# Optimization experiments

Hardware: AMD Instinct MI355X
Metric: run time of the kernel (lower is better)

## Reference

```python
import jax, jax.numpy as jnp
import numpy as np

B, Q, A, D, K = 64, 256, 256, 256, 16

def setup_inputs() -> dict:
    key = jax.random.key(0)
    k1, k2, k3, k4, k5 = jax.random.split(key, 5)
    batch_q_em = jax.random.normal(k1, (B, Q, D), dtype=jnp.float32)
    batch_da_em = jax.random.normal(k2, (B, A, D), dtype=jnp.float32)
    # xavier_uniform-style init for parameters
    lim_w = float(np.sqrt(6.0 / (D + D)))
    w = jax.random.uniform(k3, (K, D, D), minval=-lim_w, maxval=lim_w, dtype=jnp.float32)
    lim_V = float(np.sqrt(6.0 / (K + 2 * D)))
    V = jax.random.uniform(k4, (K, 2 * D), minval=-lim_V, maxval=lim_V, dtype=jnp.float32)
    lim_b = float(np.sqrt(6.0 / 2))
    b = jax.random.uniform(k5, (K, 1, 1), minval=-lim_b, maxval=lim_b, dtype=jnp.float32)
    return {"batch_q_em": batch_q_em, "batch_da_em": batch_da_em, "w": w, "V": V, "b": b}

def reference(batch_q_em, batch_da_em, w, V, b):
    Dd = batch_q_em.shape[-1]
    # bilinear term: q_i^T W_k d_j  -> [B, K, Q, A]
    first = jnp.einsum('bqd,kde,bae->bkqa', batch_q_em, w, batch_da_em)
    # linear term: V_k @ concat(q_i, d_j) == V_q @ q_i + V_d @ d_j (broadcast add)
    Vq, Vd = V[:, :Dd], V[:, Dd:]
    mid = (jnp.einsum('kd,bqd->bkq', Vq, batch_q_em)[:, :, :, None]
           + jnp.einsum('kd,bad->bka', Vd, batch_da_em)[:, :, None, :])
    return jax.nn.sigmoid(first + mid + b[None])  # b broadcasts as [1,K,1,1]
```

## Files before the change

kernel.cpp:

```cpp
#include <hip/hip_runtime.h>

typedef _Float16 h8  __attribute__((ext_vector_type(8)));
typedef _Float16 h4v __attribute__((ext_vector_type(4)));
typedef float    f32x4 __attribute__((ext_vector_type(4)));

#define QSTR 264

__global__ __launch_bounds__(256, 3)
void ntn_fused(const float* __restrict__ qg, const float* __restrict__ dg,
               const float* __restrict__ wg, const float* __restrict__ Vg,
               const float* __restrict__ bg, float* __restrict__ og)
{
    __shared__ __align__(16) _Float16 rA[64 * QSTR];
    __shared__ __align__(16) _Float16 rB[256 * 40];

    const int tid  = threadIdx.x;
    const int wv   = tid >> 6;
    const int lane = tid & 63;
    const int quad = lane >> 4;
    const int l15  = lane & 15;

    const int bid = blockIdx.x;
    const int qt = bid & 3, kk = (bid >> 2) & 15, bb = bid >> 6;

    const float* wk = wg + kk * 65536;
    const float* qb = qg + (bb * 256 + qt * 64) * 256;
    const float* db = dg + bb * 65536;
    const float* Vq = Vg + kk * 512;
    const float* Vd = Vq + 256;
    const float  bk = bg[kk];

    for (int r = 0; r < 16; ++r) {
        int f  = r * 256 + tid;
        int qq = f >> 6;
        int d4 = (f & 63) << 2;
        f32x4 v = *(const f32x4*)&qb[qq * 256 + d4];
        h4v h;
        h[0] = (_Float16)v[0]; h[1] = (_Float16)v[1];
        h[2] = (_Float16)v[2]; h[3] = (_Float16)v[3];
        *(h4v*)&rA[qq * QSTR + d4] = h;
    }

    const f32x4 zero = {0.f, 0.f, 0.f, 0.f};
    f32x4 acc[4][4];
    #pragma unroll
    for (int mt = 0; mt < 4; ++mt)
        #pragma unroll
        for (int nt = 0; nt < 4; ++nt) acc[mt][nt] = zero;

    const int e0  = (tid & 63) << 2;
    const int d0g = tid >> 6;

    for (int dc = 0; dc < 8; ++dc) {
        f32x4 Ld[8];
        #pragma unroll
        for (int r = 0; r < 8; ++r)
            Ld[r] = *(const f32x4*)&wk[(dc * 32 + d0g * 8 + r) * 256 + e0];
        #pragma unroll
        for (int i = 0; i < 4; ++i) {
            h8 hv;
            #pragma unroll
            for (int r = 0; r < 8; ++r) hv[r] = (_Float16)Ld[r][i];
            int e   = e0 + i;
            int grp = d0g ^ ((e >> 2) & 3);
            *(h8*)&rB[e * 32 + (grp << 3)] = hv;
        }
        __syncthreads();

        h8 af[4], bf[4];
        #pragma unroll
        for (int mt = 0; mt < 4; ++mt)
            af[mt] = *(const h8*)&rA[(mt * 16 + l15) * QSTR + dc * 32 + quad * 8];
        #pragma unroll
        for (int nt = 0; nt < 4; ++nt) {
            int n   = wv * 64 + nt * 16 + l15;
            int grp = quad ^ ((n >> 2) & 3);
            bf[nt] = *(const h8*)&rB[n * 32 + (grp << 3)];
        }
        #pragma unroll
        for (int mt = 0; mt < 4; ++mt)
            #pragma unroll
            for (int nt = 0; nt < 4; ++nt)
                acc[mt][nt] = __builtin_amdgcn_mfma_f32_16x16x32_f16(
                    af[mt], bf[nt], acc[mt][nt], 0, 0, 0);
        __syncthreads();
    }

    {
        float vqp = 0.f;
        int qq = tid & 63, seg = tid >> 6;
        for (int j = seg * 64; j < seg * 64 + 64; j += 8) {
            h8 hv = *(const h8*)&rA[qq * QSTR + j];
            #pragma unroll
            for (int u = 0; u < 8; ++u) vqp += (float)hv[u] * Vq[j + u];
        }
        ((float*)rB)[tid] = vqp;
    }
    __syncthreads();

    float vq_r = 0.f;
    if (tid < 64) {
        const float* fB = (const float*)rB;
        vq_r = fB[tid] + fB[tid + 64] + fB[tid + 128] + fB[tid + 192];
    }
    #pragma unroll
    for (int mt = 0; mt < 4; ++mt)
        #pragma unroll
        for (int nt = 0; nt < 4; ++nt) {
            int e = wv * 64 + nt * 16 + l15;
            #pragma unroll
            for (int reg = 0; reg < 4; ++reg) {
                int q = mt * 16 + quad * 4 + reg;
                rA[q * QSTR + e] = (_Float16)acc[mt][nt][reg];
            }
        }
    __syncthreads();

    #pragma unroll
    for (int mt = 0; mt < 4; ++mt)
        #pragma unroll
        for (int nt = 0; nt < 4; ++nt) acc[mt][nt] = zero;

    float vd_r = 0.f;
    for (int ec = 0; ec < 8; ++ec) {
        for (int r = 0; r < 8; ++r) {
            int f  = r * 256 + tid;
            int a  = f >> 3;
            int e4 = (f & 7) << 2;
            f32x4 v = *(const f32x4*)&db[a * 256 + ec * 32 + e4];
            h4v h;
            h[0] = (_Float16)v[0]; h[1] = (_Float16)v[1];
            h[2] = (_Float16)v[2]; h[3] = (_Float16)v[3];
            *(h4v*)&rB[a * 40 + e4] = h;
        }
        __syncthreads();

        #pragma unroll
        for (int j = 0; j < 32; j += 8) {
            h8 hv = *(const h8*)&rB[tid * 40 + j];
            #pragma unroll
            for (int u = 0; u < 8; ++u) vd_r += (float)hv[u] * Vd[ec * 32 + j + u];
        }

        h8 af[4], bf[4];
        #pragma unroll
        for (int mt = 0; mt < 4; ++mt)
            af[mt] = *(const h8*)&rA[(mt * 16 + l15) * QSTR + ec * 32 + quad * 8];
        #pragma unroll
        for (int nt = 0; nt < 4; ++nt)
            bf[nt] = *(const h8*)&rB[(wv * 64 + nt * 16 + l15) * 40 + quad * 8];
        #pragma unroll
        for (int mt = 0; mt < 4; ++mt)
            #pragma unroll
            for (int nt = 0; nt < 4; ++nt)
                acc[mt][nt] = __builtin_amdgcn_mfma_f32_16x16x32_f16(
                    af[mt], bf[nt], acc[mt][nt], 0, 0, 0);
        __syncthreads();
    }

    {
        float* fB = (float*)rB;
        if (tid < 64) fB[tid] = vq_r;
        fB[64 + tid] = vd_r;
    }
    __syncthreads();

    {
        const float* vql = (const float*)rB;
        const float* vdl = vql + 64;
        float* ob = og + ((bb * 16 + kk) * 256 + qt * 64) * 256;
        #pragma unroll
        for (int mt = 0; mt < 4; ++mt)
            #pragma unroll
            for (int nt = 0; nt < 4; ++nt) {
                int a = wv * 64 + nt * 16 + l15;
                float va = vdl[a];
                #pragma unroll
                for (int reg = 0; reg < 4; ++reg) {
                    int q = mt * 16 + quad * 4 + reg;
                    float x = acc[mt][nt][reg] + vql[q] + va + bk;
                    ob[q * 256 + a] = 1.0f / (1.0f + __expf(-x));
                }
            }
    }
}

extern "C" void kernel_launch(void* const* d_in, const int* in_sizes, int n_in,
                              void* d_out, int out_size, void* d_ws, size_t ws_size,
                              hipStream_t stream) {
    (void)in_sizes; (void)n_in; (void)d_ws; (void)ws_size; (void)out_size;
    const float* qg = (const float*)d_in[0];
    const float* dg = (const float*)d_in[1];
    const float* wg = (const float*)d_in[2];
    const float* Vg = (const float*)d_in[3];
    const float* bg = (const float*)d_in[4];
    float* og = (float*)d_out;
    ntn_fused<<<dim3(4096), dim3(256), 0, stream>>>(qg, dg, wg, Vg, bg, og);
}
```

Baseline: 471.6 us.

## Pre-convert inputs to swizzled fp16 in workspace and stream tiles via global_load_lds

Adds prep kernels that convert q, d and w to fp16 in pre-swizzled layouts in the workspace once per call, and a separate kernel that precomputes the Vq/Vd linear terms. The hot kernel then loads tiles straight into LDS with global_load_lds, avoiding repeated fp32 loads, conversions and transposes in each of the 4096 blocks. It also uses an XOR-swizzled unpadded LDS layout, rcp for the sigmoid and nontemporal output stores. The cost is four extra launches plus workspace traffic, and a fallback to the old kernel when the workspace is too small.

Measured after the change: 377.4 us. -20.0%, faster.

```diff
diff --git a/kernel.cpp b/kernel.cpp
--- a/kernel.cpp
+++ b/kernel.cpp
@@ -4,15 +4,137 @@
 typedef _Float16 h4v __attribute__((ext_vector_type(4)));
 typedef float    f32x4 __attribute__((ext_vector_type(4)));
 
-#define QSTR 264
+#define WS_W_OFF   0u
+#define WS_Q_OFF   (2u<<20)
+#define WS_D_OFF   (10u<<20)
+#define WS_VQ_OFF  (18u<<20)
+#define WS_VD_OFF  (22u<<20)
+#define WS_NEED    (26u<<20)
+
+__device__ __forceinline__ void gld16(const void* g, void* l) {
+    __builtin_amdgcn_global_load_lds(
+        (const __attribute__((address_space(1))) unsigned int*)g,
+        (__attribute__((address_space(3))) unsigned int*)l, 16, 0, 0);
+}
+
+
+__global__ void prep_q(const float* __restrict__ qg, _Float16* __restrict__ qs) {
+    int t0 = blockIdx.x * 256 + threadIdx.x;
+    #pragma unroll
+    for (int r = 0; r < 4; ++r) {
+        int s   = r * 131072 + t0;
+        int row = s >> 5;
+        int g   = s & 31;
+        int src = row * 256 + ((g ^ (row & 31)) << 3);
+        f32x4 v0 = *(const f32x4*)&qg[src];
+        f32x4 v1 = *(const f32x4*)&qg[src + 4];
+        h8 h;
+        #pragma unroll
+        for (int i = 0; i < 4; ++i) { h[i] = (_Float16)v0[i]; h[4 + i] = (_Float16)v1[i]; }
+        *(h8*)&qs[s * 8] = h;
+    }
+}
+
+__global__ void prep_da(const float* __restrict__ dg, _Float16* __restrict__ das) {
+    int t0 = blockIdx.x * 256 + threadIdx.x;
+    #pragma unroll
+    for (int r = 0; r < 4; ++r) {
+        int s    = r * 131072 + t0;
+        int cidx = s >> 10;
+        int sl   = s & 1023;
+        int b = cidx >> 3, ec = cidx & 7;
+        int a2 = sl >> 3, g = sl & 7;
+        int u  = g ^ (a2 & 7);
+        int a  = a2 * 2 + (u >> 2);
+        int e  = ec * 32 + (u & 3) * 8;
+        const float* src = dg + b * 65536 + a * 256 + e;
+        f32x4 v0 = *(const f32x4*)&src[0];
+        f32x4 v1 = *(const f32x4*)&src[4];
+        h8 h;
+        #pragma unroll
+        for (int i = 0; i < 4; ++i) { h[i] = (_Float16)v0[i]; h[4 + i] = (_Float16)v1[i]; }
+        *(h8*)&das[s * 8] = h;
+    }
+}
+
+__global__ void prep_w(const float* __restrict__ wg, _Float16* __restrict__ wsw) {
+    __shared__ float lt[32 * 256];
+    int tid = threadIdx.x;
+    int k = blockIdx.x >> 3, dc = blockIdx.x & 7;
+    const float* src = wg + k * 65536 + dc * 32 * 256;
+    #pragma unroll
+    for (int r = 0; r < 8; ++r) {
+        int idx = r * 256 + tid;
+        int d = idx >> 6, e4 = (idx & 63) << 2;
+        *(f32x4*)&lt[d * 256 + e4] = *(const f32x4*)&src[d * 256 + e4];
+    }
+    __syncthreads();
+    #pragma unroll
+    for (int r = 0; r < 4; ++r) {
+        int sl = r * 256 + tid;
+        int e2 = sl >> 3, g = sl & 7;
+        int u  = g ^ (e2 & 7);
+        int e  = e2 * 2 + (u >> 2);
+        int dp = (u & 3) * 8;
+        h8 h;
+        #pragma unroll
+        for (int j = 0; j < 8; ++j) h[j] = (_Float16)lt[(dp + j) * 256 + e];
+        *(h8*)&wsw[(blockIdx.x * 1024 + sl) * 8] = h;
+    }
+}
+
+__global__ void prep_v(const float* __restrict__ qg, const float* __restrict__ dg,
+                       const float* __restrict__ Vg, float* __restrict__ vq,
+                       float* __restrict__ vd) {
+    __shared__ float Vl[16 * 256];
+    int blk = blockIdx.x, t = threadIdx.x;
+    int mode = blk >> 8;
+    int b = (blk & 255) >> 2, qc = blk & 3;
+    const float* srcb = (mode ? dg : qg) + b * 65536;
+    float* outp = mode ? vd : vq;
+    int voff = mode ? 256 : 0;
+    #pragma unroll
+    for (int r = 0; r < 4; ++r) {
+        int idx = r * 256 + t;
+        int k = idx >> 6, d4 = (idx & 63) << 2;
+        *(f32x4*)&Vl[k * 256 + d4] = *(const f32x4*)&Vg[k * 512 + voff + d4];
+    }
+    __syncthreads();
+    int ql = t & 63, seg = t >> 6;
+    const float* row = srcb + (qc * 64 + ql) * 256 + seg * 64;
+    float s[16];
+    #pragma unroll
+    for (int k = 0; k < 16; ++k) s[k] = 0.f;
+    for (int d4 = 0; d4 < 64; d4 += 4) {
+        f32x4 rv = *(const f32x4*)&row[d4];
+        #pragma unroll
+        for (int k = 0; k < 16; ++k) {
+            f32x4 vv = *(const f32x4*)&Vl[k * 256 + seg * 64 + d4];
+            s[k] += rv[0] * vv[0] + rv[1] * vv[1] + rv[2] * vv[2] + rv[3] * vv[3];
+        }
+    }
+    __syncthreads();
+    #pragma unroll
+    for (int k = 0; k < 16; ++k) Vl[(seg * 16 + k) * 64 + ql] = s[k];
+    __syncthreads();
+    #pragma unroll
+    for (int i = 0; i < 4; ++i) {
+        int idx = i * 256 + t;
+        int k = idx >> 6, qq = idx & 63;
+        float sum = Vl[(0 * 16 + k) * 64 + qq] + Vl[(1 * 16 + k) * 64 + qq] +
+                    Vl[(2 * 16 + k) * 64 + qq] + Vl[(3 * 16 + k) * 64 + qq];
+        outp[(b * 16 + k) * 256 + qc * 64 + qq] = sum;
+    }
+}
 
 __global__ __launch_bounds__(256, 3)
-void ntn_fused(const float* __restrict__ qg, const float* __restrict__ dg,
-               const float* __restrict__ wg, const float* __restrict__ Vg,
-               const float* __restrict__ bg, float* __restrict__ og)
+void ntn_hot(const _Float16* __restrict__ qs, const _Float16* __restrict__ das,
+             const _Float16* __restrict__ wsw, const float* __restrict__ vq,
+             const float* __restrict__ vd, const float* __restrict__ bg,
+             float* __restrict__ og)
 {
-    __shared__ __align__(16) _Float16 rA[64 * QSTR];
-    __shared__ __align__(16) _Float16 rB[256 * 40];
+    __shared__ __align__(16) _Float16 rA[64 * 256];
+    __shared__ __align__(16) _Float16 wB[256 * 32];
 
     const int tid  = threadIdx.x;
     const int wv   = tid >> 6;
@@ -23,34 +145,177 @@
     const int bid = blockIdx.x;
     const int qt = bid & 3, kk = (bid >> 2) & 15, bb = bid >> 6;
 
+    const char* qsrc = (const char*)(qs + (bb * 256 + qt * 64) * 256);
+    #pragma unroll
+    for (int r = 0; r < 8; ++r) {
+        int base = r * 256 + wv * 64;
+        gld16(qsrc + (base + lane) * 16, (char*)rA + base * 16);
+    }
+
+    const char* wsrc = (const char*)wsw + kk * 8 * 16384;
+    const char* dsrc = (const char*)das + bb * 8 * 16384;
+
+    #pragma unroll
+    for (int r = 0; r < 4; ++r) {
+        int base = r * 256 + wv * 64;
+        gld16(wsrc + (base + lane) * 16, (char*)wB + base * 16);
+    }
+    __syncthreads();
+
+    int rowAo[4], rswz[4];
+    #pragma unroll
+    for (int mt = 0; mt < 4; ++mt) {
+        int row = mt * 16 + l15;
+        rowAo[mt] = row * 256;
+        rswz[mt]  = row & 31;
+    }
+    int addrB[4];
+    #pragma unroll
+    for (int nt = 0; nt < 4; ++nt) {
+        int e = wv * 64 + nt * 16 + l15;
+        addrB[nt] = (e >> 1) * 64 + (((((e & 1) << 2) + quad) ^ ((e >> 1) & 7)) << 3);
+    }
+
+    const f32x4 zero = {0.f, 0.f, 0.f, 0.f};
+    f32x4 acc[4][4];
+    #pragma unroll
+    for (int mt = 0; mt < 4; ++mt)
+        #pragma unroll
+        for (int nt = 0; nt < 4; ++nt) acc[mt][nt] = zero;
+
+    for (int dc = 0; dc < 8; ++dc) {
+        h8 af[4], bf[4];
+        #pragma unroll
+        for (int mt = 0; mt < 4; ++mt)
+            af[mt] = *(const h8*)&rA[rowAo[mt] + ((((dc << 2) + quad) ^ rswz[mt]) << 3)];
+        #pragma unroll
+        for (int nt = 0; nt < 4; ++nt)
+            bf[nt] = *(const h8*)&wB[addrB[nt]];
+        #pragma unroll
+        for (int mt = 0; mt < 4; ++mt)
+            #pragma unroll
+            for (int nt = 0; nt < 4; ++nt)
+                acc[mt][nt] = __builtin_amdgcn_mfma_f32_16x16x32_f16(
+                    af[mt], bf[nt], acc[mt][nt], 0, 0, 0);
+        __syncthreads();
+        if (dc < 7) {
+            #pragma unroll
+            for (int r = 0; r < 4; ++r) {
+                int base = r * 256 + wv * 64;
+                gld16(wsrc + (dc + 1) * 16384 + (base + lane) * 16, (char*)wB + base * 16);
+            }
+            __syncthreads();
+        }
+    }
+
+    #pragma unroll
+    for (int r = 0; r < 4; ++r) {
+        int base = r * 256 + wv * 64;
+        gld16(dsrc + (base + lane) * 16, (char*)wB + base * 16);
+    }
+    #pragma unroll
+    for (int mt = 0; mt < 4; ++mt)
+        #pragma unroll
+        for (int nt = 0; nt < 4; ++nt) {
+            int e = wv * 64 + nt * 16 + l15;
+            #pragma unroll
+            for (int reg = 0; reg < 4; ++reg) {
+                int q = mt * 16 + quad * 4 + reg;
+                rA[q * 256 + ((((e >> 3) ^ (q & 31)) << 3) | (e & 7))] =
+                    (_Float16)acc[mt][nt][reg];
+            }
+        }
+    #pragma unroll
+    for (int mt = 0; mt < 4; ++mt)
+        #pragma unroll
+        for (int nt = 0; nt < 4; ++nt) acc[mt][nt] = zero;
+    __syncthreads();
+
+    for (int ec = 0; ec < 8; ++ec) {
+        h8 af[4], bf[4];
+        #pragma unroll
+        for (int mt = 0; mt < 4; ++mt)
+            af[mt] = *(const h8*)&rA[rowAo[mt] + ((((ec << 2) + quad) ^ rswz[mt]) << 3)];
+        #pragma unroll
+        for (int nt = 0; nt < 4; ++nt)
+            bf[nt] = *(const h8*)&wB[addrB[nt]];
+        #pragma unroll
+        for (int mt = 0; mt < 4; ++mt)
+            #pragma unroll
+            for (int nt = 0; nt < 4; ++nt)
+                acc[mt][nt] = __builtin_amdgcn_mfma_f32_16x16x32_f16(
+                    af[mt], bf[nt], acc[mt][nt], 0, 0, 0);
+        __syncthreads();
+        if (ec < 7) {
+            #pragma unroll
+            for (int r = 0; r < 4; ++r) {
+                int base = r * 256 + wv * 64;
+                gld16(dsrc + (ec + 1) * 16384 + (base + lane) * 16, (char*)wB + base * 16);
+            }
+            __syncthreads();
+        }
+    }
+
+    const float* vqp = vq + ((bb * 16 + kk) << 8) + qt * 64;
+    const float* vdp = vd + ((bb * 16 + kk) << 8);
+    const float  bk  = bg[kk];
+    float vdr[4];
+    #pragma unroll
+    for (int nt = 0; nt < 4; ++nt) vdr[nt] = vdp[wv * 64 + nt * 16 + l15];
+    float* ob = og + (((bb * 16 + kk) * 256 + qt * 64) << 8);
+    #pragma unroll
+    for (int mt = 0; mt < 4; ++mt) {
+        float vqv[4];
+        #pragma unroll
+        for (int r = 0; r < 4; ++r) vqv[r] = vqp[mt * 16 + quad * 4 + r];
+        #pragma unroll
+        for (int nt = 0; nt < 4; ++nt)
+            #pragma unroll
+            for (int r = 0; r < 4; ++r) {
+                float x = acc[mt][nt][r] + vqv[r] + vdr[nt] + bk;
+                float y = __builtin_amdgcn_rcpf(1.0f + __expf(-x));
+                __builtin_nontemporal_store(
+                    y, &ob[(mt * 16 + quad * 4 + r) * 256 + wv * 64 + nt * 16 + l15]);
+            }
+    }
+}
+
+#define QSTR 264
+__global__ __launch_bounds__(256, 3)
+void ntn_fused_fb(const float* __restrict__ qg, const float* __restrict__ dg,
+                  const float* __restrict__ wg, const float* __restrict__ Vg,
+                  const float* __restrict__ bg, float* __restrict__ og)
+{
+    __shared__ __align__(16) _Float16 rA[64 * QSTR];
+    __shared__ __align__(16) _Float16 rB[256 * 40];
+    const int tid  = threadIdx.x;
+    const int wv   = tid >> 6;
+    const int lane = tid & 63;
+    const int quad = lane >> 4;
+    const int l15  = lane & 15;
+    const int bid = blockIdx.x;
+    const int qt = bid & 3, kk = (bid >> 2) & 15, bb = bid >> 6;
     const float* wk = wg + kk * 65536;
     const float* qb = qg + (bb * 256 + qt * 64) * 256;
     const float* db = dg + bb * 65536;
     const float* Vq = Vg + kk * 512;
     const float* Vd = Vq + 256;
     const float  bk = bg[kk];
-
     for (int r = 0; r < 16; ++r) {
-        int f  = r * 256 + tid;
-        int qq = f >> 6;
-        int d4 = (f & 63) << 2;
+        int f = r * 256 + tid;
+        int qq = f >> 6, d4 = (f & 63) << 2;
         f32x4 v = *(const f32x4*)&qb[qq * 256 + d4];
-        h4v h;
-        h[0] = (_Float16)v[0]; h[1] = (_Float16)v[1];
-        h[2] = (_Float16)v[2]; h[3] = (_Float16)v[3];
+        h4v h; h[0]=(_Float16)v[0]; h[1]=(_Float16)v[1]; h[2]=(_Float16)v[2]; h[3]=(_Float16)v[3];
         *(h4v*)&rA[qq * QSTR + d4] = h;
     }
-
-    const f32x4 zero = {0.f, 0.f, 0.f, 0.f};
+    const f32x4 zero = {0.f,0.f,0.f,0.f};
     f32x4 acc[4][4];
     #pragma unroll
     for (int mt = 0; mt < 4; ++mt)
         #pragma unroll
         for (int nt = 0; nt < 4; ++nt) acc[mt][nt] = zero;
-
-    const int e0  = (tid & 63) << 2;
+    const int e0 = (tid & 63) << 2;
     const int d0g = tid >> 6;
-
     for (int dc = 0; dc < 8; ++dc) {
         f32x4 Ld[8];
         #pragma unroll
@@ -61,19 +326,18 @@
             h8 hv;
             #pragma unroll
             for (int r = 0; r < 8; ++r) hv[r] = (_Float16)Ld[r][i];
-            int e   = e0 + i;
+            int e = e0 + i;
             int grp = d0g ^ ((e >> 2) & 3);
             *(h8*)&rB[e * 32 + (grp << 3)] = hv;
         }
         __syncthreads();
-
         h8 af[4], bf[4];
         #pragma unroll
         for (int mt = 0; mt < 4; ++mt)
             af[mt] = *(const h8*)&rA[(mt * 16 + l15) * QSTR + dc * 32 + quad * 8];
         #pragma unroll
         for (int nt = 0; nt < 4; ++nt) {
-            int n   = wv * 64 + nt * 16 + l15;
+            int n = wv * 64 + nt * 16 + l15;
             int grp = quad ^ ((n >> 2) & 3);
             bf[nt] = *(const h8*)&rB[n * 32 + (grp << 3)];
         }
@@ -81,11 +345,9 @@
         for (int mt = 0; mt < 4; ++mt)
             #pragma unroll
             for (int nt = 0; nt < 4; ++nt)
-                acc[mt][nt] = __builtin_amdgcn_mfma_f32_16x16x32_f16(
-                    af[mt], bf[nt], acc[mt][nt], 0, 0, 0);
-        __syncthreads();
-    }
-
+                acc[mt][nt] = __builtin_amdgcn_mfma_f32_16x16x32_f16(af[mt], bf[nt], acc[mt][nt], 0, 0, 0);
+        __syncthreads();
+    }
     {
         float vqp = 0.f;
         int qq = tid & 63, seg = tid >> 6;
@@ -97,7 +359,6 @@
         ((float*)rB)[tid] = vqp;
     }
     __syncthreads();
-
     float vq_r = 0.f;
     if (tid < 64) {
         const float* fB = (const float*)rB;
@@ -115,33 +376,26 @@
             }
         }
     __syncthreads();
-
     #pragma unroll
     for (int mt = 0; mt < 4; ++mt)
         #pragma unroll
         for (int nt = 0; nt < 4; ++nt) acc[mt][nt] = zero;
-
     float vd_r = 0.f;
     for (int ec = 0; ec < 8; ++ec) {
         for (int r = 0; r < 8; ++r) {
-            int f  = r * 256 + tid;
-            int a  = f >> 3;
-            int e4 = (f & 7) << 2;
+            int f = r * 256 + tid;
+            int a = f >> 3, e4 = (f & 7) << 2;
             f32x4 v = *(const f32x4*)&db[a * 256 + ec * 32 + e4];
-            h4v h;
-            h[0] = (_Float16)v[0]; h[1] = (_Float16)v[1];
-            h[2] = (_Float16)v[2]; h[3] = (_Float16)v[3];
+            h4v h; h[0]=(_Float16)v[0]; h[1]=(_Float16)v[1]; h[2]=(_Float16)v[2]; h[3]=(_Float16)v[3];
             *(h4v*)&rB[a * 40 + e4] = h;
         }
         __syncthreads();
-
         #pragma unroll
         for (int j = 0; j < 32; j += 8) {
             h8 hv = *(const h8*)&rB[tid * 40 + j];
             #pragma unroll
             for (int u = 0; u < 8; ++u) vd_r += (float)hv[u] * Vd[ec * 32 + j + u];
         }
-
         h8 af[4], bf[4];
         #pragma unroll
         for (int mt = 0; mt < 4; ++mt)
@@ -153,18 +407,15 @@
         for (int mt = 0; mt < 4; ++mt)
             #pragma unroll
             for (int nt = 0; nt < 4; ++nt)
-                acc[mt][nt] = __builtin_amdgcn_mfma_f32_16x16x32_f16(
-                    af[mt], bf[nt], acc[mt][nt], 0, 0, 0);
-        __syncthreads();
-    }
-
+                acc[mt][nt] = __builtin_amdgcn_mfma_f32_16x16x32_f16(af[mt], bf[nt], acc[mt][nt], 0, 0, 0);
+        __syncthreads();
+    }
     {
         float* fB = (float*)rB;
         if (tid < 64) fB[tid] = vq_r;
         fB[64 + tid] = vd_r;
     }
     __syncthreads();
-
     {
         const float* vql = (const float*)rB;
         const float* vdl = vql + 64;
@@ -188,12 +439,27 @@
 extern "C" void kernel_launch(void* const* d_in, const int* in_sizes, int n_in,
                               void* d_out, int out_size, void* d_ws, size_t ws_size,
                               hipStream_t stream) {
-    (void)in_sizes; (void)n_in; (void)d_ws; (void)ws_size; (void)out_size;
+    (void)in_sizes; (void)n_in; (void)out_size;
     const float* qg = (const float*)d_in[0];
     const float* dg = (const float*)d_in[1];
     const float* wg = (const float*)d_in[2];
     const float* Vg = (const float*)d_in[3];
     const float* bg = (const float*)d_in[4];
     float* og = (float*)d_out;
-    ntn_fused<<<dim3(4096), dim3(256), 0, stream>>>(qg, dg, wg, Vg, bg, og);
-}
+
+    if (ws_size >= (size_t)WS_NEED) {
+        char* ws = (char*)d_ws;
+        _Float16* wsw = (_Float16*)(ws + WS_W_OFF);
+        _Float16* qsp = (_Float16*)(ws + WS_Q_OFF);
+        _Float16* dsp = (_Float16*)(ws + WS_D_OFF);
+        float*    vqp = (float*)(ws + WS_VQ_OFF);
+        float*    vdp = (float*)(ws + WS_VD_OFF);
+        prep_q <<<512, 256, 0, stream>>>(qg, qsp);
+        prep_da<<<512, 256, 0, stream>>>(dg, dsp);
+        prep_w <<<128, 256, 0, stream>>>(wg, wsw);
+        prep_v <<<512, 256, 0, stream>>>(qg, dg, Vg, vqp, vdp);
+        ntn_hot<<<4096, 256, 0, stream>>>(qsp, dsp, wsw, vqp, vdp, bg, og);
+    } else {
+        ntn_fused_fb<<<4096, 256, 0, stream>>>(qg, dg, wg, Vg, bg, og);
+    }
+}
```
